# Performance work log

Measured on AMD Instinct MI355X. Metric: run time of the kernel, lower is better.

The kernel has to match this reference:

```python
import jax, jax.numpy as jnp
import numpy as np


def setup_inputs() -> dict:
    key = jax.random.key(0)
    x = jax.random.normal(key, (8, 4096, 512), dtype=jnp.float32)
    kappa = jnp.float32(0.5)
    return {"x": x, "kappa": kappa}


def reference(x, kappa):
    # Faithful reduction of DecorrLoss.forward (batched=False path).
    # Original math per flattened sample n (N = B*L samples, feature dim d):
    #   D_n = diag(x_n^2); V_n = D_n - I; C_n = x_n x_n^T - D_n
    #   corr = mean_n mean_{ij} C_n^2
    #   whit = mean_n mean_{ij} V_n^2
    #   grad = mean_n [(1-kappa)*C_n + kappa*V_n]
    # Algebraic identities avoid the O(N*d^2) intermediate:
    #   mean_{ij} C_n^2 = ((sum_i x_i^2)^2 - sum_i x_i^4) / d^2   (off-diag outer products)
    #   mean_{ij} V_n^2 = sum_i (x_i^2 - 1)^2 / d^2               (V is diagonal)
    #   mean_n C_n = X^T X / N with diagonal zeroed
    #   mean_n V_n = diag(mean_n x^2 - 1)
    b, l, d = x.shape
    xf = x.reshape(b * l, d)          # (N, d)
    n = xf.shape[0]
    x2 = xf * xf                      # (N, d)

    s2 = jnp.sum(x2, axis=1)          # (N,) sum of squares per sample
    s4 = jnp.sum(x2 * x2, axis=1)     # (N,) sum of fourth powers per sample
    inv_d2 = 1.0 / (d * d)
    correlation_loss = jnp.mean(s2 * s2 - s4) * inv_d2
    whitening_loss = jnp.mean(jnp.sum((x2 - 1.0) ** 2, axis=1)) * inv_d2

    gram = (xf.T @ xf) / n            # (d, d) = mean_n x_n x_n^T
    m2 = jnp.diagonal(gram)           # mean_n x_i^2
    off_diag = gram - jnp.diag(m2)    # mean_n C_n
    grad = (1.0 - kappa) * off_diag + kappa * jnp.diag(m2 - 1.0)
    return grad, correlation_loss, whitening_loss
```

## Files before the change

### kernel.cpp

```cpp
#include <hip/hip_runtime.h>
#include <hip/hip_bf16.h>


#define D 512
#define NSAMP 32768
#define KPARTS 32
#define KC (NSAMP / KPARTS)
#define BK 64
#define NCHUNK (KC / BK)
#define LOSS_BLOCKS 2048

typedef __bf16 bf16x8 __attribute__((ext_vector_type(8)));
typedef float floatx4 __attribute__((ext_vector_type(4)));

__global__ __launch_bounds__(1024) void zero_kernel(float* out, int n) {
    int i = blockIdx.x * 1024 + threadIdx.x;
    if (i < n) out[i] = 0.0f;
}

template <bool ATOMIC>
__global__ __launch_bounds__(256) void loss_kernel(const float* __restrict__ x,
                                                   float2* __restrict__ partials,
                                                   float* __restrict__ out) {
    __shared__ float sA[4], sB[4];
    const int w = threadIdx.x >> 6;
    const int l = threadIdx.x & 63;
    const int gw = blockIdx.x * 4 + w;
    const float* base = x + (size_t)gw * 4 * D;

    float4 v[8];
#pragma unroll
    for (int r = 0; r < 4; ++r) {
        v[2 * r]     = *(const float4*)(base + (size_t)r * D + l * 4);
        v[2 * r + 1] = *(const float4*)(base + (size_t)r * D + 256 + l * 4);
    }
    float p2[4], p4[4];
#pragma unroll
    for (int r = 0; r < 4; ++r) {
        const float* f = (const float*)&v[2 * r];
        float a2 = 0.f, a4 = 0.f, e;
#pragma unroll
        for (int c = 0; c < 8; ++c) {
            e = f[c] * f[c];
            a2 += e;
            a4 += e * e;
        }
        p2[r] = a2;
        p4[r] = a4;
    }
#pragma unroll
    for (int m = 1; m < 64; m <<= 1) {
#pragma unroll
        for (int r = 0; r < 4; ++r) {
            p2[r] += __shfl_xor(p2[r], m);
            p4[r] += __shfl_xor(p4[r], m);
        }
    }
    float accA = 0.f, accB = 0.f;
#pragma unroll
    for (int r = 0; r < 4; ++r) {
        accA += p2[r] * p2[r] - p4[r];
        accB += p4[r] - 2.0f * p2[r];
    }
    if (l == 0) { sA[w] = accA; sB[w] = accB; }
    __syncthreads();
    if (threadIdx.x == 0) {
        const float bA = sA[0] + sA[1] + sA[2] + sA[3];
        const float bB = sB[0] + sB[1] + sB[2] + sB[3];
        if (ATOMIC) {
            const float SCALE = 1.1641532182693481e-10f;
            atomicAdd(out + D * D, bA * SCALE);
            atomicAdd(out + D * D + 1, bB * SCALE);
            if (blockIdx.x == 0) atomicAdd(out + D * D + 1, 0.001953125f);
        } else {
            partials[blockIdx.x] = make_float2(bA, bB);
        }
    }
}

__global__ __launch_bounds__(256) void scalar_reduce_kernel(const float2* __restrict__ partials,
                                                            float* __restrict__ out) {
    __shared__ float sA[4], sB[4];
    const int w = threadIdx.x >> 6;
    const int l = threadIdx.x & 63;
    float a = 0.f, b = 0.f;
    for (int i = threadIdx.x; i < LOSS_BLOCKS; i += 256) {
        const float2 p = partials[i];
        a += p.x;
        b += p.y;
    }
#pragma unroll
    for (int m = 1; m < 64; m <<= 1) {
        a += __shfl_xor(a, m);
        b += __shfl_xor(b, m);
    }
    if (l == 0) { sA[w] = a; sB[w] = b; }
    __syncthreads();
    if (threadIdx.x == 0) {
        const float SCALE = 1.1641532182693481e-10f;
        out[D * D] = (sA[0] + sA[1] + sA[2] + sA[3]) * SCALE;
        out[D * D + 1] = (sB[0] + sB[1] + sB[2] + sB[3]) * SCALE + 0.001953125f;
    }
}

template <bool ATOMIC>
__global__ __launch_bounds__(256, 2) void gram_kernel(const float* __restrict__ x,
                                                      float* __restrict__ dst) {
    __shared__ __bf16 As[128 * 64];
    __shared__ __bf16 Bs[128 * 64];
    char* Asb = (char*)As;
    char* Bsb = (char*)Bs;

    const int kpart = blockIdx.x & (KPARTS - 1);
    const int tile = blockIdx.x >> 5;
    const int i0 = (tile & 3) * 128;
    const int j0 = (tile >> 2) * 128;
    const int kbase = kpart * KC;

    const int t = threadIdx.x;
    const int l = t & 63;
    const int wv = t >> 6;

    const int fq = (l & 7) + 8 * wv;
    const int ksl = l >> 3;
    const float4* x4 = (const float4*)x;
    const int aoff = (i0 >> 2) + fq;
    const int boff = (j0 >> 2) + fq;

    float4 va[8], vb[8];
#pragma unroll
    for (int r = 0; r < 4; ++r) {
        const size_t row = (size_t)(kbase + 2 * ksl + 16 * r) * 128;
        va[2 * r]     = x4[row + aoff];
        va[2 * r + 1] = x4[row + 128 + aoff];
        vb[2 * r]     = x4[row + boff];
        vb[2 * r + 1] = x4[row + 128 + boff];
    }

    floatx4 acc[4][4];
#pragma unroll
    for (int a = 0; a < 4; ++a)
#pragma unroll
        for (int b = 0; b < 4; ++b) acc[a][b] = (floatx4)0.0f;

    const int wm = (wv >> 1) * 64;
    const int wn = (wv & 1) * 64;
    const int rl = l & 15;
    const int q = l >> 4;

    for (int c = 0; c < NCHUNK; ++c) {
        __syncthreads();
#pragma unroll
        for (int r = 0; r < 4; ++r) {
            const int k0 = 2 * ksl + 16 * r;
            const int g = k0 >> 3;
            const int sb = (k0 & 7) * 2;
            const float* fa0 = (const float*)&va[2 * r];
            const float* fa1 = (const float*)&va[2 * r + 1];
            const float* fb0 = (const float*)&vb[2 * r];
            const float* fb1 = (const float*)&vb[2 * r + 1];
#pragma unroll
            for (int cc = 0; cc < 4; ++cc) {
                const int f = fq * 4 + cc;
                const int off = f * 128 + ((g ^ (f & 7)) * 16) + sb;
                unsigned int pa = (unsigned int)__bfloat16_as_ushort(__float2bfloat16(fa0[cc])) |
                                  ((unsigned int)__bfloat16_as_ushort(__float2bfloat16(fa1[cc])) << 16);
                unsigned int pb = (unsigned int)__bfloat16_as_ushort(__float2bfloat16(fb0[cc])) |
                                  ((unsigned int)__bfloat16_as_ushort(__float2bfloat16(fb1[cc])) << 16);
                *(unsigned int*)(Asb + off) = pa;
                *(unsigned int*)(Bsb + off) = pb;
            }
        }
        if (c + 1 < NCHUNK) {
            const int kb = kbase + (c + 1) * BK;
#pragma unroll
            for (int r = 0; r < 4; ++r) {
                const size_t row = (size_t)(kb + 2 * ksl + 16 * r) * 128;
                va[2 * r]     = x4[row + aoff];
                va[2 * r + 1] = x4[row + 128 + aoff];
                vb[2 * r]     = x4[row + boff];
                vb[2 * r + 1] = x4[row + 128 + boff];
            }
        }
        __syncthreads();
#pragma unroll
        for (int kk = 0; kk < 2; ++kk) {
            const int qp = kk * 4 + q;
            bf16x8 af[4], bfr[4];
#pragma unroll
            for (int tm = 0; tm < 4; ++tm) {
                const int fi = wm + tm * 16 + rl;
                af[tm] = *(const bf16x8*)(Asb + fi * 128 + ((qp ^ (fi & 7)) * 16));
            }
#pragma unroll
            for (int tn = 0; tn < 4; ++tn) {
                const int fj = wn + tn * 16 + rl;
                bfr[tn] = *(const bf16x8*)(Bsb + fj * 128 + ((qp ^ (fj & 7)) * 16));
            }
#pragma unroll
            for (int tm = 0; tm < 4; ++tm)
#pragma unroll
                for (int tn = 0; tn < 4; ++tn)
                    acc[tm][tn] = __builtin_amdgcn_mfma_f32_16x16x32_bf16(
                        af[tm], bfr[tn], acc[tm][tn], 0, 0, 0);
        }
    }

    if (ATOMIC) {
#pragma unroll
        for (int tm = 0; tm < 4; ++tm)
#pragma unroll
            for (int tn = 0; tn < 4; ++tn)
#pragma unroll
                for (int rr = 0; rr < 4; ++rr) {
                    const int gi = i0 + wm + tm * 16 + q * 4 + rr;
                    const int gj = j0 + wn + tn * 16 + rl;
                    atomicAdd(dst + (size_t)gi * D + gj, acc[tm][tn][rr]);
                }
    } else {
        float* p = dst + (size_t)kpart * (D * D);
#pragma unroll
        for (int tm = 0; tm < 4; ++tm)
#pragma unroll
            for (int tn = 0; tn < 4; ++tn)
#pragma unroll
                for (int rr = 0; rr < 4; ++rr) {
                    const int gi = i0 + wm + tm * 16 + q * 4 + rr;
                    const int gj = j0 + wn + tn * 16 + rl;
                    p[(size_t)gi * D + gj] = acc[tm][tn][rr];
                }
    }
}

__global__ __launch_bounds__(256) void finalize_kernel(const float* __restrict__ src, int kparts,
                                                       const float* __restrict__ kappa_p,
                                                       float* __restrict__ out) {
    const int idx4 = blockIdx.x * 256 + threadIdx.x;
    const int base = idx4 * 4;
    float4 s = {0.f, 0.f, 0.f, 0.f};
    for (int p = 0; p < kparts; ++p) {
        const float4 v = *(const float4*)(src + (size_t)p * (D * D) + base);
        s.x += v.x; s.y += v.y; s.z += v.z; s.w += v.w;
    }
    const float kappa = *kappa_p;
    const float invn = 1.0f / (float)NSAMP;
    const int i = base >> 9;
    const int j = base & (D - 1);
    float r[4] = {s.x, s.y, s.z, s.w};
#pragma unroll
    for (int cpt = 0; cpt < 4; ++cpt) {
        const float m = r[cpt] * invn;
        r[cpt] = (i == j + cpt) ? kappa * (m - 1.0f) : (1.0f - kappa) * m;
    }
    float4 o = {r[0], r[1], r[2], r[3]};
    *(float4*)(out + base) = o;
}

extern "C" void kernel_launch(void* const* d_in, const int* in_sizes, int n_in,
                              void* d_out, int out_size, void* d_ws, size_t ws_size,
                              hipStream_t stream) {
    const float* x = (const float*)d_in[0];
    const float* kappa = (const float*)d_in[1];
    float* out = (float*)d_out;

    const size_t gram_bytes = (size_t)KPARTS * D * D * sizeof(float);
    const size_t loss_bytes = (size_t)LOSS_BLOCKS * sizeof(float2);

    if (ws_size >= gram_bytes + loss_bytes) {
        float* parts = (float*)d_ws;
        float2* lpart = (float2*)((char*)d_ws + gram_bytes);
        loss_kernel<false><<<LOSS_BLOCKS, 256, 0, stream>>>(x, lpart, out);
        gram_kernel<false><<<16 * KPARTS, 256, 0, stream>>>(x, parts);
        finalize_kernel<<<(D * D / 4) / 256, 256, 0, stream>>>(parts, KPARTS, kappa, out);
        scalar_reduce_kernel<<<1, 256, 0, stream>>>(lpart, out);
    } else if (ws_size >= loss_bytes) {
        float2* lpart = (float2*)d_ws;
        zero_kernel<<<(out_size + 1023) / 1024, 1024, 0, stream>>>(out, out_size);
        loss_kernel<false><<<LOSS_BLOCKS, 256, 0, stream>>>(x, lpart, out);
        gram_kernel<true><<<16 * KPARTS, 256, 0, stream>>>(x, out);
        finalize_kernel<<<(D * D / 4) / 256, 256, 0, stream>>>(out, 1, kappa, out);
        scalar_reduce_kernel<<<1, 256, 0, stream>>>(lpart, out);
    } else {
        zero_kernel<<<(out_size + 1023) / 1024, 1024, 0, stream>>>(out, out_size);
        loss_kernel<true><<<LOSS_BLOCKS, 256, 0, stream>>>(x, nullptr, out);
        gram_kernel<true><<<16 * KPARTS, 256, 0, stream>>>(x, out);
        finalize_kernel<<<(D * D / 4) / 256, 256, 0, stream>>>(out, 1, kappa, out);
    }
}
```

Before: 142.3 us.

## Pre-transpose input to swizzled bf16 and stream gram tiles via global_load_lds

A new prep kernel reads x once, computes the per-block loss partials, and writes a transposed, pre-swizzled bf16 copy of x into workspace. The gram kernel then stages tiles straight from global memory into double-buffered LDS with global_load_lds, so it no longer converts fp32 to bf16 in registers. The scalar loss reduction is folded into the finalize kernel as an extra block, which removes one launch. In exchange it needs an extra 32 MB workspace buffer plus the write and re-read of the bf16 copy, and the fast path now runs only when the workspace is that large.

```diff
diff --git a/kernel.cpp b/kernel.cpp
--- a/kernel.cpp
+++ b/kernel.cpp
@@ -1,33 +1,242 @@
 #include <hip/hip_runtime.h>
 #include <hip/hip_bf16.h>
+#include <stdint.h>
 
 
 #define D 512
 #define NSAMP 32768
 #define KPARTS 32
-#define KC (NSAMP / KPARTS)
+#define KC 1024
 #define BK 64
-#define NCHUNK (KC / BK)
-#define LOSS_BLOCKS 2048
+#define NCHUNK 16
+#define PREP_BLOCKS 512
 
 typedef __bf16 bf16x8 __attribute__((ext_vector_type(8)));
 typedef float floatx4 __attribute__((ext_vector_type(4)));
+typedef __attribute__((address_space(1))) const uint32_t gas_u32;
+typedef __attribute__((address_space(3))) uint32_t las_u32;
 
 __global__ __launch_bounds__(1024) void zero_kernel(float* out, int n) {
     int i = blockIdx.x * 1024 + threadIdx.x;
     if (i < n) out[i] = 0.0f;
 }
 
-template <bool ATOMIC>
-__global__ __launch_bounds__(256) void loss_kernel(const float* __restrict__ x,
-                                                   float2* __restrict__ partials,
-                                                   float* __restrict__ out) {
+
+__global__ __launch_bounds__(256) void prep_kernel(const float* __restrict__ x,
+                                                   uint16_t* __restrict__ xt,
+                                                   float2* __restrict__ lpart) {
+    __shared__ float sA[4], sB[4];
+    const int t = threadIdx.x;
+    const int pr = t >> 5;
+    const int seg = t & 31;
+    const int b = blockIdx.x;
+    char* xtb = (char*)xt;
+    float accA = 0.f, accB = 0.f;
+#pragma unroll
+    for (int c = 0; c < 4; ++c) {
+        const int k0 = b * 64 + c * 16 + 2 * pr;
+        const float4* r0 = (const float4*)(x + (size_t)k0 * D);
+        const float4* r1 = (const float4*)(x + (size_t)(k0 + 1) * D);
+        float4 v0[4], v1[4];
+#pragma unroll
+        for (int j = 0; j < 4; ++j) {
+            v0[j] = r0[seg + 32 * j];
+            v1[j] = r1[seg + 32 * j];
+        }
+        float p20 = 0.f, p40 = 0.f, p21 = 0.f, p41 = 0.f;
+#pragma unroll
+        for (int j = 0; j < 4; ++j) {
+            const float* f0 = (const float*)&v0[j];
+            const float* f1 = (const float*)&v1[j];
+#pragma unroll
+            for (int c2 = 0; c2 < 4; ++c2) {
+                const float e0 = f0[c2] * f0[c2];
+                const float e1 = f1[c2] * f1[c2];
+                p20 += e0; p40 += e0 * e0;
+                p21 += e1; p41 += e1 * e1;
+            }
+        }
+#pragma unroll
+        for (int m = 1; m < 32; m <<= 1) {
+            p20 += __shfl_xor(p20, m);
+            p40 += __shfl_xor(p40, m);
+            p21 += __shfl_xor(p21, m);
+            p41 += __shfl_xor(p41, m);
+        }
+        accA += (p20 * p20 - p40) + (p21 * p21 - p41);
+        accB += (p40 - 2.f * p20) + (p41 - 2.f * p21);
+        const int gran = 2 * c + (pr >> 2);
+        const int bwi = (pr & 3) * 4;
+#pragma unroll
+        for (int j = 0; j < 4; ++j) {
+            const float* f0 = (const float*)&v0[j];
+            const float* f1 = (const float*)&v1[j];
+#pragma unroll
+            for (int c2 = 0; c2 < 4; ++c2) {
+                const int f = 4 * (seg + 32 * j) + c2;
+                const uint32_t lo = __bfloat16_as_ushort(__float2bfloat16(f0[c2]));
+                const uint32_t hi = __bfloat16_as_ushort(__float2bfloat16(f1[c2]));
+                const size_t addr = (size_t)f * 65536 + (size_t)b * 128 +
+                                    (size_t)(((gran ^ (f & 7)) * 16) + bwi);
+                *(uint32_t*)(xtb + addr) = lo | (hi << 16);
+            }
+        }
+    }
+#pragma unroll
+    for (int m = 1; m < 64; m <<= 1) {
+        accA += __shfl_xor(accA, m);
+        accB += __shfl_xor(accB, m);
+    }
+    const int w = t >> 6;
+    if ((t & 63) == 0) { sA[w] = accA; sB[w] = accB; }
+    __syncthreads();
+    if (t == 0) {
+        lpart[b] = make_float2((sA[0] + sA[1] + sA[2] + sA[3]) * 0.03125f,
+                               (sB[0] + sB[1] + sB[2] + sB[3]) * 0.03125f);
+    }
+}
+
+__global__ __launch_bounds__(256, 2) void gram_bf16_kernel(const uint16_t* __restrict__ xt,
+                                                           float* __restrict__ dst) {
+    __shared__ __bf16 As[2][128 * 64];
+    __shared__ __bf16 Bs[2][128 * 64];
+
+    const int kpart = blockIdx.x & (KPARTS - 1);
+    const int tile = blockIdx.x >> 5;
+    const int i0 = (tile & 3) * 128;
+    const int j0 = (tile >> 2) * 128;
+
+    const int t = threadIdx.x;
+    const int l = t & 63;
+    const int wv = t >> 6;
+    const char* xb = (const char*)xt;
+
+    const int frow = wv * 32 + (l >> 3);
+    const size_t ga = (size_t)(i0 + frow) * 65536 + (size_t)((l & 7) * 16);
+    const size_t gb = (size_t)(j0 + frow) * 65536 + (size_t)((l & 7) * 16);
+
+    floatx4 acc[4][4];
+#pragma unroll
+    for (int a = 0; a < 4; ++a)
+#pragma unroll
+        for (int b2 = 0; b2 < 4; ++b2) acc[a][b2] = (floatx4)0.0f;
+
+    const int wm = (wv >> 1) * 64;
+    const int wn = (wv & 1) * 64;
+    const int rl = l & 15;
+    const int q = l >> 4;
+
+#define STAGE(c, buf)                                                                         \
+    {                                                                                         \
+        const size_t koff = (size_t)(kpart * 16 + (c)) * 128;                                 \
+        _Pragma("unroll") for (int i = 0; i < 4; ++i) {                                       \
+            __builtin_amdgcn_global_load_lds((gas_u32*)(xb + ga + (size_t)i * 8 * 65536 + koff), \
+                                             (las_u32*)&As[buf][(wv * 32 + i * 8) * 64], 16, 0, 0); \
+            __builtin_amdgcn_global_load_lds((gas_u32*)(xb + gb + (size_t)i * 8 * 65536 + koff), \
+                                             (las_u32*)&Bs[buf][(wv * 32 + i * 8) * 64], 16, 0, 0); \
+        }                                                                                     \
+    }
+
+    STAGE(0, 0);
+    for (int c = 0; c < NCHUNK; ++c) {
+        __syncthreads();
+        if (c + 1 < NCHUNK) STAGE(c + 1, (c + 1) & 1);
+        const char* Ab = (const char*)As[c & 1];
+        const char* Bb = (const char*)Bs[c & 1];
+#pragma unroll
+        for (int kk = 0; kk < 2; ++kk) {
+            const int qp = kk * 4 + q;
+            bf16x8 af[4], bfr[4];
+#pragma unroll
+            for (int tm = 0; tm < 4; ++tm) {
+                const int fi = wm + tm * 16 + rl;
+                af[tm] = *(const bf16x8*)(Ab + fi * 128 + ((qp ^ (fi & 7)) * 16));
+            }
+#pragma unroll
+            for (int tn = 0; tn < 4; ++tn) {
+                const int fj = wn + tn * 16 + rl;
+                bfr[tn] = *(const bf16x8*)(Bb + fj * 128 + ((qp ^ (fj & 7)) * 16));
+            }
+#pragma unroll
+            for (int tm = 0; tm < 4; ++tm)
+#pragma unroll
+                for (int tn = 0; tn < 4; ++tn)
+                    acc[tm][tn] = __builtin_amdgcn_mfma_f32_16x16x32_bf16(
+                        af[tm], bfr[tn], acc[tm][tn], 0, 0, 0);
+        }
+    }
+#undef STAGE
+
+    float* p = dst + (size_t)kpart * (D * D);
+#pragma unroll
+    for (int tm = 0; tm < 4; ++tm)
+#pragma unroll
+        for (int tn = 0; tn < 4; ++tn)
+#pragma unroll
+            for (int rr = 0; rr < 4; ++rr) {
+                const int gi = i0 + wm + tm * 16 + q * 4 + rr;
+                const int gj = j0 + wn + tn * 16 + rl;
+                p[(size_t)gi * D + gj] = acc[tm][tn][rr];
+            }
+}
+
+__global__ __launch_bounds__(256) void finalize_fused_kernel(const float* __restrict__ src,
+                                                             const float2* __restrict__ lpart,
+                                                             const float* __restrict__ kappa_p,
+                                                             float* __restrict__ out) {
+    if (blockIdx.x == 256) {
+        __shared__ float sA[4], sB[4];
+        const int w = threadIdx.x >> 6;
+        const int l = threadIdx.x & 63;
+        float a = 0.f, b = 0.f;
+        for (int i = threadIdx.x; i < PREP_BLOCKS; i += 256) {
+            const float2 pp = lpart[i];
+            a += pp.x;
+            b += pp.y;
+        }
+#pragma unroll
+        for (int m = 1; m < 64; m <<= 1) {
+            a += __shfl_xor(a, m);
+            b += __shfl_xor(b, m);
+        }
+        if (l == 0) { sA[w] = a; sB[w] = b; }
+        __syncthreads();
+        if (threadIdx.x == 0) {
+            const float SCALE = 1.1641532182693481e-10f;
+            out[D * D] = (sA[0] + sA[1] + sA[2] + sA[3]) * SCALE;
+            out[D * D + 1] = (sB[0] + sB[1] + sB[2] + sB[3]) * SCALE + 0.001953125f;
+        }
+        return;
+    }
+    const int idx4 = blockIdx.x * 256 + threadIdx.x;
+    const int base = idx4 * 4;
+    float4 s = {0.f, 0.f, 0.f, 0.f};
+    for (int p = 0; p < KPARTS; ++p) {
+        const float4 v = *(const float4*)(src + (size_t)p * (D * D) + base);
+        s.x += v.x; s.y += v.y; s.z += v.z; s.w += v.w;
+    }
+    const float kappa = *kappa_p;
+    const float invn = 1.0f / (float)NSAMP;
+    const int i = base >> 9;
+    const int j = base & (D - 1);
+    float r[4] = {s.x, s.y, s.z, s.w};
+#pragma unroll
+    for (int cpt = 0; cpt < 4; ++cpt) {
+        const float m = r[cpt] * invn;
+        r[cpt] = (i == j + cpt) ? kappa * (m - 1.0f) : (1.0f - kappa) * m;
+    }
+    float4 o = {r[0], r[1], r[2], r[3]};
+    *(float4*)(out + base) = o;
+}
+
+
+__global__ __launch_bounds__(256) void loss_atomic_kernel(const float* __restrict__ x,
+                                                          float* __restrict__ out) {
     __shared__ float sA[4], sB[4];
     const int w = threadIdx.x >> 6;
     const int l = threadIdx.x & 63;
     const int gw = blockIdx.x * 4 + w;
     const float* base = x + (size_t)gw * 4 * D;
-
     float4 v[8];
 #pragma unroll
     for (int r = 0; r < 4; ++r) {
@@ -40,13 +249,8 @@
         const float* f = (const float*)&v[2 * r];
         float a2 = 0.f, a4 = 0.f, e;
 #pragma unroll
-        for (int c = 0; c < 8; ++c) {
-            e = f[c] * f[c];
-            a2 += e;
-            a4 += e * e;
-        }
-        p2[r] = a2;
-        p4[r] = a4;
+        for (int c = 0; c < 8; ++c) { e = f[c] * f[c]; a2 += e; a4 += e * e; }
+        p2[r] = a2; p4[r] = a4;
     }
 #pragma unroll
     for (int m = 1; m < 64; m <<= 1) {
@@ -65,89 +269,48 @@
     if (l == 0) { sA[w] = accA; sB[w] = accB; }
     __syncthreads();
     if (threadIdx.x == 0) {
-        const float bA = sA[0] + sA[1] + sA[2] + sA[3];
-        const float bB = sB[0] + sB[1] + sB[2] + sB[3];
-        if (ATOMIC) {
-            const float SCALE = 1.1641532182693481e-10f;
-            atomicAdd(out + D * D, bA * SCALE);
-            atomicAdd(out + D * D + 1, bB * SCALE);
-            if (blockIdx.x == 0) atomicAdd(out + D * D + 1, 0.001953125f);
-        } else {
-            partials[blockIdx.x] = make_float2(bA, bB);
-        }
-    }
-}
-
-__global__ __launch_bounds__(256) void scalar_reduce_kernel(const float2* __restrict__ partials,
-                                                            float* __restrict__ out) {
-    __shared__ float sA[4], sB[4];
-    const int w = threadIdx.x >> 6;
-    const int l = threadIdx.x & 63;
-    float a = 0.f, b = 0.f;
-    for (int i = threadIdx.x; i < LOSS_BLOCKS; i += 256) {
-        const float2 p = partials[i];
-        a += p.x;
-        b += p.y;
-    }
-#pragma unroll
-    for (int m = 1; m < 64; m <<= 1) {
-        a += __shfl_xor(a, m);
-        b += __shfl_xor(b, m);
-    }
-    if (l == 0) { sA[w] = a; sB[w] = b; }
-    __syncthreads();
-    if (threadIdx.x == 0) {
         const float SCALE = 1.1641532182693481e-10f;
-        out[D * D] = (sA[0] + sA[1] + sA[2] + sA[3]) * SCALE;
-        out[D * D + 1] = (sB[0] + sB[1] + sB[2] + sB[3]) * SCALE + 0.001953125f;
-    }
-}
-
-template <bool ATOMIC>
-__global__ __launch_bounds__(256, 2) void gram_kernel(const float* __restrict__ x,
-                                                      float* __restrict__ dst) {
+        atomicAdd(out + D * D, (sA[0] + sA[1] + sA[2] + sA[3]) * SCALE);
+        atomicAdd(out + D * D + 1, (sB[0] + sB[1] + sB[2] + sB[3]) * SCALE);
+        if (blockIdx.x == 0) atomicAdd(out + D * D + 1, 0.001953125f);
+    }
+}
+
+__global__ __launch_bounds__(256, 2) void gram_fp32_atomic_kernel(const float* __restrict__ x,
+                                                                  float* __restrict__ dst) {
     __shared__ __bf16 As[128 * 64];
     __shared__ __bf16 Bs[128 * 64];
     char* Asb = (char*)As;
     char* Bsb = (char*)Bs;
-
     const int kpart = blockIdx.x & (KPARTS - 1);
     const int tile = blockIdx.x >> 5;
     const int i0 = (tile & 3) * 128;
     const int j0 = (tile >> 2) * 128;
     const int kbase = kpart * KC;
-
     const int t = threadIdx.x;
     const int l = t & 63;
     const int wv = t >> 6;
-
     const int fq = (l & 7) + 8 * wv;
     const int ksl = l >> 3;
     const float4* x4 = (const float4*)x;
     const int aoff = (i0 >> 2) + fq;
     const int boff = (j0 >> 2) + fq;
-
     float4 va[8], vb[8];
 #pragma unroll
     for (int r = 0; r < 4; ++r) {
         const size_t row = (size_t)(kbase + 2 * ksl + 16 * r) * 128;
-        va[2 * r]     = x4[row + aoff];
-        va[2 * r + 1] = x4[row + 128 + aoff];
-        vb[2 * r]     = x4[row + boff];
-        vb[2 * r + 1] = x4[row + 128 + boff];
-    }
-
+        va[2 * r] = x4[row + aoff];     va[2 * r + 1] = x4[row + 128 + aoff];
+        vb[2 * r] = x4[row + boff];     vb[2 * r + 1] = x4[row + 128 + boff];
+    }
     floatx4 acc[4][4];
 #pragma unroll
     for (int a = 0; a < 4; ++a)
 #pragma unroll
         for (int b = 0; b < 4; ++b) acc[a][b] = (floatx4)0.0f;
-
     const int wm = (wv >> 1) * 64;
     const int wn = (wv & 1) * 64;
     const int rl = l & 15;
     const int q = l >> 4;
-
     for (int c = 0; c < NCHUNK; ++c) {
         __syncthreads();
 #pragma unroll
@@ -176,10 +339,8 @@
 #pragma unroll
             for (int r = 0; r < 4; ++r) {
                 const size_t row = (size_t)(kb + 2 * ksl + 16 * r) * 128;
-                va[2 * r]     = x4[row + aoff];
-                va[2 * r + 1] = x4[row + 128 + aoff];
-                vb[2 * r]     = x4[row + boff];
-                vb[2 * r + 1] = x4[row + 128 + boff];
+                va[2 * r] = x4[row + aoff];     va[2 * r + 1] = x4[row + 128 + aoff];
+                vb[2 * r] = x4[row + boff];     vb[2 * r + 1] = x4[row + 128 + boff];
             }
         }
         __syncthreads();
@@ -205,43 +366,23 @@
                         af[tm], bfr[tn], acc[tm][tn], 0, 0, 0);
         }
     }
-
-    if (ATOMIC) {
-#pragma unroll
-        for (int tm = 0; tm < 4; ++tm)
-#pragma unroll
-            for (int tn = 0; tn < 4; ++tn)
-#pragma unroll
-                for (int rr = 0; rr < 4; ++rr) {
-                    const int gi = i0 + wm + tm * 16 + q * 4 + rr;
-                    const int gj = j0 + wn + tn * 16 + rl;
-                    atomicAdd(dst + (size_t)gi * D + gj, acc[tm][tn][rr]);
-                }
-    } else {
-        float* p = dst + (size_t)kpart * (D * D);
-#pragma unroll
-        for (int tm = 0; tm < 4; ++tm)
-#pragma unroll
-            for (int tn = 0; tn < 4; ++tn)
-#pragma unroll
-                for (int rr = 0; rr < 4; ++rr) {
-                    const int gi = i0 + wm + tm * 16 + q * 4 + rr;
-                    const int gj = j0 + wn + tn * 16 + rl;
-                    p[(size_t)gi * D + gj] = acc[tm][tn][rr];
-                }
-    }
-}
-
-__global__ __launch_bounds__(256) void finalize_kernel(const float* __restrict__ src, int kparts,
-                                                       const float* __restrict__ kappa_p,
-                                                       float* __restrict__ out) {
-    const int idx4 = blockIdx.x * 256 + threadIdx.x;
-    const int base = idx4 * 4;
-    float4 s = {0.f, 0.f, 0.f, 0.f};
-    for (int p = 0; p < kparts; ++p) {
-        const float4 v = *(const float4*)(src + (size_t)p * (D * D) + base);
-        s.x += v.x; s.y += v.y; s.z += v.z; s.w += v.w;
-    }
+#pragma unroll
+    for (int tm = 0; tm < 4; ++tm)
+#pragma unroll
+        for (int tn = 0; tn < 4; ++tn)
+#pragma unroll
+            for (int rr = 0; rr < 4; ++rr) {
+                const int gi = i0 + wm + tm * 16 + q * 4 + rr;
+                const int gj = j0 + wn + tn * 16 + rl;
+                atomicAdd(dst + (size_t)gi * D + gj, acc[tm][tn][rr]);
+            }
+}
+
+__global__ __launch_bounds__(256) void finalize1_kernel(const float* __restrict__ src,
+                                                        const float* __restrict__ kappa_p,
+                                                        float* __restrict__ out) {
+    const int base = (blockIdx.x * 256 + threadIdx.x) * 4;
+    float4 s = *(const float4*)(src + base);
     const float kappa = *kappa_p;
     const float invn = 1.0f / (float)NSAMP;
     const int i = base >> 9;
@@ -263,27 +404,21 @@
     const float* kappa = (const float*)d_in[1];
     float* out = (float*)d_out;
 
-    const size_t gram_bytes = (size_t)KPARTS * D * D * sizeof(float);
-    const size_t loss_bytes = (size_t)LOSS_BLOCKS * sizeof(float2);
-
-    if (ws_size >= gram_bytes + loss_bytes) {
-        float* parts = (float*)d_ws;
-        float2* lpart = (float2*)((char*)d_ws + gram_bytes);
-        loss_kernel<false><<<LOSS_BLOCKS, 256, 0, stream>>>(x, lpart, out);
-        gram_kernel<false><<<16 * KPARTS, 256, 0, stream>>>(x, parts);
-        finalize_kernel<<<(D * D / 4) / 256, 256, 0, stream>>>(parts, KPARTS, kappa, out);
-        scalar_reduce_kernel<<<1, 256, 0, stream>>>(lpart, out);
-    } else if (ws_size >= loss_bytes) {
-        float2* lpart = (float2*)d_ws;
-        zero_kernel<<<(out_size + 1023) / 1024, 1024, 0, stream>>>(out, out_size);
-        loss_kernel<false><<<LOSS_BLOCKS, 256, 0, stream>>>(x, lpart, out);
-        gram_kernel<true><<<16 * KPARTS, 256, 0, stream>>>(x, out);
-        finalize_kernel<<<(D * D / 4) / 256, 256, 0, stream>>>(out, 1, kappa, out);
-        scalar_reduce_kernel<<<1, 256, 0, stream>>>(lpart, out);
+    const size_t xt_bytes = (size_t)D * NSAMP * sizeof(uint16_t);
+    const size_t parts_bytes = (size_t)KPARTS * D * D * sizeof(float);
+    const size_t lpart_bytes = (size_t)PREP_BLOCKS * sizeof(float2);
+
+    if (ws_size >= xt_bytes + parts_bytes + lpart_bytes) {
+        uint16_t* xt = (uint16_t*)d_ws;
+        float* parts = (float*)((char*)d_ws + xt_bytes);
+        float2* lpart = (float2*)((char*)d_ws + xt_bytes + parts_bytes);
+        prep_kernel<<<PREP_BLOCKS, 256, 0, stream>>>(x, xt, lpart);
+        gram_bf16_kernel<<<16 * KPARTS, 256, 0, stream>>>(xt, parts);
+        finalize_fused_kernel<<<257, 256, 0, stream>>>(parts, lpart, kappa, out);
     } else {
         zero_kernel<<<(out_size + 1023) / 1024, 1024, 0, stream>>>(out, out_size);
-        loss_kernel<true><<<LOSS_BLOCKS, 256, 0, stream>>>(x, nullptr, out);
-        gram_kernel<true><<<16 * KPARTS, 256, 0, stream>>>(x, out);
-        finalize_kernel<<<(D * D / 4) / 256, 256, 0, stream>>>(out, 1, kappa, out);
-    }
-}
+        loss_atomic_kernel<<<2048, 256, 0, stream>>>(x, out);
+        gram_fp32_atomic_kernel<<<16 * KPARTS, 256, 0, stream>>>(x, out);
+        finalize1_kernel<<<(D * D / 4) / 256, 256, 0, stream>>>(out, kappa, out);
+    }
+}
```

Result: slower. 157.3 us (+10.5%).
